# Kernel optimization log

Hardware: AMD Instinct MI355X
Metric: run time of the kernel (lower is better)

The kernel has to match this reference:

```python
import jax, jax.numpy as jnp
import numpy as np

SEQ, B, IN, H, L = 1024, 64, 256, 512, 2
EPS = 1e-5


def setup_inputs() -> dict:
    key = jax.random.key(0)
    ks = jax.random.split(key, 4)
    x = jax.random.normal(ks[0], (SEQ, B, IN), dtype=jnp.float32)
    h0 = jnp.zeros((L, B, H), dtype=jnp.float32)
    c0 = jnp.zeros((L, B, H), dtype=jnp.float32)
    # torch Linear weight layout: [4*H, in_features]
    W0 = jax.random.normal(ks[1], (4 * H, IN + H), dtype=jnp.float32) * 0.05
    b0 = jnp.zeros((4 * H,), dtype=jnp.float32)
    W1 = jax.random.normal(ks[2], (4 * H, H + H), dtype=jnp.float32) * 0.05
    b1 = jnp.zeros((4 * H,), dtype=jnp.float32)
    g0 = jnp.ones((H,), dtype=jnp.float32)
    beta0 = jnp.zeros((H,), dtype=jnp.float32)
    g1 = jnp.ones((H,), dtype=jnp.float32)
    beta1 = jnp.zeros((H,), dtype=jnp.float32)
    return {"x": x, "h0": h0, "c0": c0, "W0": W0, "b0": b0, "g0": g0,
            "beta0": beta0, "W1": W1, "b1": b1, "g1": g1, "beta1": beta1}


def _layer_norm(z, g, b):
    mu = jnp.mean(z, axis=-1, keepdims=True)
    var = jnp.mean(jnp.square(z - mu), axis=-1, keepdims=True)
    return (z - mu) * jax.lax.rsqrt(var + EPS) * g + b


def _cell(inp, h, c, W, b, g, beta):
    # gates: [B, 4H] via Linear on concat(x, h)
    gates = jnp.concatenate([inp, h], axis=-1) @ W.T + b
    i_t, f_t, o_t, cand = jnp.split(gates, 4, axis=-1)
    i_t = jax.nn.sigmoid(i_t)
    f_t = jax.nn.sigmoid(f_t)
    o_t = jax.nn.sigmoid(o_t)
    cand = jnp.tanh(cand)
    c_new = i_t * cand + f_t * c
    h_new = o_t * jnp.tanh(_layer_norm(c_new, g, beta))
    return h_new, c_new


def reference(x, h0, c0, W0, b0, g0, beta0, W1, b1, g1, beta1):
    def step(carry, xt):
        ha, ca, hb, cb = carry
        ha, ca = _cell(xt, ha, ca, W0, b0, g0, beta0)
        hb, cb = _cell(ha, hb, cb, W1, b1, g1, beta1)
        return (ha, ca, hb, cb), hb

    carry0 = (h0[0], c0[0], h0[1], c0[1])
    (ha, ca, hb, cb), outputs = jax.lax.scan(step, carry0, x)
    h_final = jnp.stack([ha, hb])  # [L, B, H]
    c_final = jnp.stack([ca, cb])
    return outputs, h_final, c_final
```

## Files before the change

kernel.cpp:

```cpp
#include <hip/hip_runtime.h>


typedef short  s16x8 __attribute__((ext_vector_type(8)));
typedef float  f32x4 __attribute__((ext_vector_type(4)));
typedef float  f32x2 __attribute__((ext_vector_type(2)));
typedef unsigned short u16;
typedef unsigned int   u32;

constexpr int kSeq = 1024;

constexpr size_t OF_FLAGS = 0;
constexpr size_t OF_PART0 = 1024;
constexpr size_t OF_PART1 = 33792;
constexpr size_t OF_HA    = 66560;
constexpr size_t OF_HB    = 197632;
constexpr size_t OF_W0S   = 328704;
constexpr size_t OF_W1S   = 3474432;
constexpr size_t OF_XBF   = 7668736;
constexpr size_t WS_NEED  = OF_XBF + 33554432;

constexpr size_t OUT_HFIN = (size_t)kSeq * 64 * 512;
constexpr size_t OUT_CFIN = OUT_HFIN + 2 * 64 * 512;

__device__ __forceinline__ u16 f2bf(float f) {
  u32 u = __float_as_uint(f);
  return (u16)((u + 0x7fffu + ((u >> 16) & 1u)) >> 16);
}

__device__ __forceinline__ void ldg16_coh(s16x8& d, const void* p) {
  asm volatile("global_load_dwordx4 %0, %1, off sc0 sc1" : "=v"(d) : "v"(p) : "memory");
}
__device__ __forceinline__ void ldg16f_coh(f32x4& d, const void* p) {
  asm volatile("global_load_dwordx4 %0, %1, off sc0 sc1" : "=v"(d) : "v"(p) : "memory");
}
__device__ __forceinline__ void stg8_coh(float* p, float a, float b) {
  f32x2 t; t[0] = a; t[1] = b;
  asm volatile("global_store_dwordx2 %0, %1, off sc0 sc1" :: "v"(p), "v"(t) : "memory");
}
__device__ __forceinline__ void stg2_coh(u16* p, u32 v) {
  asm volatile("global_store_short %0, %1, off sc0 sc1" :: "v"(p), "v"(v) : "memory");
}
__device__ __forceinline__ void vm_wait() {
  asm volatile("s_waitcnt vmcnt(0)" ::: "memory");
  __builtin_amdgcn_sched_barrier(0);
}
__device__ __forceinline__ void waitge(u32* f, u32 tgt) {
  const int l = threadIdx.x & 63;
  while (true) {
    u32 v = __hip_atomic_load(&f[l], __ATOMIC_RELAXED, __HIP_MEMORY_SCOPE_AGENT);
    if (__all((int)(v >= tgt))) break;
    __builtin_amdgcn_s_sleep(2);
  }
}

__global__ void conv_x_k(const float* __restrict__ x, u16* __restrict__ xd, size_t n) {
  size_t i = (size_t)blockIdx.x * blockDim.x + threadIdx.x;
  size_t st = (size_t)gridDim.x * blockDim.x;
  for (; i < n; i += st) xd[i] = f2bf(x[i]);
}

__global__ void conv_w_k(const float* __restrict__ W, u16* __restrict__ Wd,
                         int KST, int Kdim) {
  int i = blockIdx.x * blockDim.x + threadIdx.x;
  if (i >= 64 * KST * 1024) return;
  int e = i & 7, lane = (i >> 3) & 63, nt = (i >> 9) & 1;
  int r = i >> 10;
  int kst = r % KST, ns = r / KST;
  int lv = nt * 16 + (lane & 15);
  int n_orig = (lv >> 3) * 512 + ns * 8 + (lv & 7);
  int k = kst * 32 + ((lane >> 4) << 3) + e;
  Wd[i] = f2bf(W[(size_t)n_orig * Kdim + k]);
}

__global__ void init_k(char* ws, const float* __restrict__ h0) {
  int i = blockIdx.x * blockDim.x + threadIdx.x;
  u32* f = (u32*)ws;
  if (i < 256) f[i] = 0u;
  ((u16*)(ws + OF_HA))[32768 + i] = f2bf(h0[i]);
  ((u16*)(ws + OF_HB))[32768 + i] = f2bf(h0[32768 + i]);
}

template <int ROLE>
__device__ __forceinline__ void team_loop(
    int ns, char* smem,
    const u16* __restrict__ xbf, const u16* __restrict__ wsw,
    u16* hA, u16* hB, float* part, u32* flags,
    const float* __restrict__ bias, const float* __restrict__ gam_,
    const float* __restrict__ bet_, const float* __restrict__ c0in,
    float* __restrict__ out)
{
  constexpr int KST = ROLE ? 32 : 24;
  const int tid = threadIdx.x;
  const int lane = tid & 63, wid = tid >> 6;
  const int arow = wid * 16 + (lane & 15);
  const int acol = (lane >> 4) << 3;
  const int b1r = tid >> 3, jl = tid & 7, b2r = b1r + 32;
  const int jg = ns * 8 + jl;

  u32* HF0 = flags;
  u32* HF1 = flags + 64;
  u32* PF  = flags + 128 + ROLE * 64;
  u32* HF  = ROLE ? HF1 : HF0;

  s16x8* wl    = (s16x8*)smem;
  float* gates = (float*)(smem + 65536);
  float* mus   = (float*)(smem + 73728);

  const u16* wbase = wsw + (size_t)ns * KST * 1024;
  for (int i = tid; i < KST * 128; i += 256)
    wl[i] = *(const s16x8*)(wbase + (size_t)i * 8);

  const float bi = bias[jg], bf_ = bias[512 + jg], bo = bias[1024 + jg], bc = bias[1536 + jg];
  const float gm = gam_[jg], bt = bet_[jg];
  float cA = c0in[(size_t)(ROLE * 64 + b1r) * 512 + jg];
  float cB = c0in[(size_t)(ROLE * 64 + b2r) * 512 + jg];
  __syncthreads();

  for (int t = 0; t < kSeq; ++t) {
    f32x4 acc0 = {0.f, 0.f, 0.f, 0.f}, acc1 = {0.f, 0.f, 0.f, 0.f};

    auto mm = [&](s16x8 av, int kst) {
      acc0 = __builtin_amdgcn_mfma_f32_16x16x32_bf16(av, wl[(kst * 2) * 64 + lane], acc0, 0, 0, 0);
      acc1 = __builtin_amdgcn_mfma_f32_16x16x32_bf16(av, wl[(kst * 2 + 1) * 64 + lane], acc1, 0, 0, 0);
    };

    if (ROLE == 0) {
      s16x8 xp[8];
      const u16* xrow = xbf + ((size_t)t * 64 + arow) * 256 + acol;
      #pragma unroll
      for (int kk = 0; kk < 8; ++kk) xp[kk] = *(const s16x8*)(xrow + kk * 32);
      if (wid == 0)      { if (t > 0)  waitge(HF0, (u32)t); }
      else if (wid == 1) { if (t >= 2) waitge(HF1, (u32)(t - 1)); }
      __syncthreads();
      s16x8 a[16];
      const u16* hrow = hA + (size_t)((t + 1) & 1) * 32768 + (size_t)arow * 512 + acol;
      #pragma unroll
      for (int kk = 0; kk < 16; ++kk) ldg16_coh(a[kk], hrow + kk * 32);
      #pragma unroll
      for (int kk = 0; kk < 8; ++kk) mm(xp[kk], kk);
      vm_wait();
      #pragma unroll
      for (int kk = 0; kk < 16; ++kk) mm(a[kk], 8 + kk);
    } else {
      if (wid == 1) { if (t > 0) waitge(HF1, (u32)t); }
      __syncthreads();
      s16x8 a[16];
      const u16* hbrow = hB + (size_t)((t + 1) & 1) * 32768 + (size_t)arow * 512 + acol;
      #pragma unroll
      for (int kk = 0; kk < 16; ++kk) ldg16_coh(a[kk], hbrow + kk * 32);
      vm_wait();
      #pragma unroll
      for (int kk = 0; kk < 16; ++kk) mm(a[kk], 16 + kk);
      if (wid == 0) waitge(HF0, (u32)(t + 1));
      __syncthreads();
      const u16* harow = hA + (size_t)(t & 1) * 32768 + (size_t)arow * 512 + acol;
      #pragma unroll
      for (int kk = 0; kk < 16; ++kk) ldg16_coh(a[kk], harow + kk * 32);
      vm_wait();
      #pragma unroll
      for (int kk = 0; kk < 16; ++kk) mm(a[kk], kk);
    }

    #pragma unroll
    for (int r = 0; r < 4; ++r) {
      const int b = wid * 16 + ((lane >> 4) << 2) + r;
      gates[b * 32 + (lane & 15)]      = acc0[r];
      gates[b * 32 + 16 + (lane & 15)] = acc1[r];
    }
    __syncthreads();

    const float giA = gates[b1r * 32 + jl] + bi;
    const float gfA = gates[b1r * 32 + 8 + jl] + bf_;
    const float goA = gates[b1r * 32 + 16 + jl] + bo;
    const float gcA = gates[b1r * 32 + 24 + jl] + bc;
    const float giB = gates[b2r * 32 + jl] + bi;
    const float gfB = gates[b2r * 32 + 8 + jl] + bf_;
    const float goB = gates[b2r * 32 + 16 + jl] + bo;
    const float gcB = gates[b2r * 32 + 24 + jl] + bc;
    const float iA = 1.f / (1.f + __expf(-giA));
    const float fA = 1.f / (1.f + __expf(-gfA));
    const float oA = 1.f / (1.f + __expf(-goA));
    const float iB = 1.f / (1.f + __expf(-giB));
    const float fB = 1.f / (1.f + __expf(-gfB));
    const float oB = 1.f / (1.f + __expf(-goB));
    const float cnA = iA * tanhf(gcA) + fA * cA;
    const float cnB = iB * tanhf(gcB) + fB * cB;
    cA = cnA; cB = cnB;

    float s1 = cnA, q1 = cnA * cnA, s2 = cnB, q2 = cnB * cnB;
    #pragma unroll
    for (int m = 1; m <= 4; m <<= 1) {
      s1 += __shfl_xor(s1, m); q1 += __shfl_xor(q1, m);
      s2 += __shfl_xor(s2, m); q2 += __shfl_xor(q2, m);
    }
    if (jl == 0) {
      stg8_coh(part + ((size_t)b1r * 64 + ns) * 2, s1, q1);
      stg8_coh(part + ((size_t)b2r * 64 + ns) * 2, s2, q2);
    }
    vm_wait();
    __syncthreads();
    if (tid == 0)
      __hip_atomic_store(&PF[ns], (u32)(t + 1), __ATOMIC_RELAXED, __HIP_MEMORY_SCOPE_AGENT);
    if (wid == 0) waitge(PF, (u32)(t + 1));
    __syncthreads();
    if (tid < 64) {
      float ssum = 0.f, qsum = 0.f;
      const float* pr = part + (size_t)tid * 128;
      #pragma unroll
      for (int bch = 0; bch < 4; ++bch) {
        f32x4 gb[8];
        #pragma unroll
        for (int i2 = 0; i2 < 8; ++i2) ldg16f_coh(gb[i2], pr + (bch * 8 + i2) * 4);
        vm_wait();
        #pragma unroll
        for (int i2 = 0; i2 < 8; ++i2) { ssum += gb[i2][0] + gb[i2][2]; qsum += gb[i2][1] + gb[i2][3]; }
      }
      const float mu = ssum * (1.f / 512.f);
      const float ms = qsum * (1.f / 512.f);
      mus[tid * 2]     = mu;
      mus[tid * 2 + 1] = rsqrtf(ms - mu * mu + 1e-5f);
    }
    __syncthreads();
    const float muA = mus[b1r * 2], rsA = mus[b1r * 2 + 1];
    const float muB = mus[b2r * 2], rsB = mus[b2r * 2 + 1];
    const float hvA = oA * tanhf((cnA - muA) * rsA * gm + bt);
    const float hvB = oB * tanhf((cnB - muB) * rsB * gm + bt);
    const u32 ha16 = f2bf(hvA), hb16 = f2bf(hvB);

    u16* hd = (ROLE ? hB : hA) + (size_t)(t & 1) * 32768;
    stg2_coh(hd + (size_t)b1r * 512 + jg, ha16);
    stg2_coh(hd + (size_t)b2r * 512 + jg, hb16);
    if (ROLE == 1) {
      out[((size_t)t * 64 + b1r) * 512 + jg] = hvA;
      out[((size_t)t * 64 + b2r) * 512 + jg] = hvB;
    }
    if (t == kSeq - 1) {
      const size_t hb_ = OUT_HFIN + (size_t)ROLE * 32768;
      const size_t cb_ = OUT_CFIN + (size_t)ROLE * 32768;
      out[hb_ + (size_t)b1r * 512 + jg] = hvA;
      out[hb_ + (size_t)b2r * 512 + jg] = hvB;
      out[cb_ + (size_t)b1r * 512 + jg] = cnA;
      out[cb_ + (size_t)b2r * 512 + jg] = cnB;
    }
    vm_wait();
    __syncthreads();
    if (tid == 0)
      __hip_atomic_store(&HF[ns], (u32)(t + 1), __ATOMIC_RELAXED, __HIP_MEMORY_SCOPE_AGENT);
  }
}

__global__ __launch_bounds__(256, 1) void lstm_persist(
    const u16* __restrict__ xbf, const u16* __restrict__ w0s, const u16* __restrict__ w1s,
    char* ws,
    const float* __restrict__ b0, const float* __restrict__ lg0, const float* __restrict__ lb0,
    const float* __restrict__ b1, const float* __restrict__ lg1, const float* __restrict__ lb1,
    const float* __restrict__ c0in, float* __restrict__ out)
{
  extern __shared__ char smem[];
  const int bid = blockIdx.x;
  u32*   flags = (u32*)(ws + OF_FLAGS);
  u16*   hA    = (u16*)(ws + OF_HA);
  u16*   hB    = (u16*)(ws + OF_HB);
  float* p0    = (float*)(ws + OF_PART0);
  float* p1    = (float*)(ws + OF_PART1);

  if (bid < 64)
    team_loop<0>(bid, smem, xbf, w0s, hA, hB, p0, flags, b0, lg0, lb0, c0in, out);
  else
    team_loop<1>(bid - 64, smem, xbf, w1s, hA, hB, p1, flags, b1, lg1, lb1, c0in, out);
}

extern "C" void kernel_launch(void* const* d_in, const int* in_sizes, int n_in,
                              void* d_out, int out_size, void* d_ws, size_t ws_size,
                              hipStream_t stream) {
  (void)in_sizes; (void)n_in; (void)out_size;
  const float* x   = (const float*)d_in[0];
  const float* h0  = (const float*)d_in[1];
  const float* c0  = (const float*)d_in[2];
  const float* W0  = (const float*)d_in[3];
  const float* b0  = (const float*)d_in[4];
  const float* g0  = (const float*)d_in[5];
  const float* be0 = (const float*)d_in[6];
  const float* W1  = (const float*)d_in[7];
  const float* b1  = (const float*)d_in[8];
  const float* g1  = (const float*)d_in[9];
  const float* be1 = (const float*)d_in[10];
  float* out = (float*)d_out;

  if (ws_size < WS_NEED) return;

  char* ws = (char*)d_ws;
  u16* w0s = (u16*)(ws + OF_W0S);
  u16* w1s = (u16*)(ws + OF_W1S);
  u16* xbf = (u16*)(ws + OF_XBF);

  hipLaunchKernelGGL(conv_x_k, dim3(2048), dim3(256), 0, stream,
                     x, xbf, (size_t)kSeq * 64 * 256);
  hipLaunchKernelGGL(conv_w_k, dim3(6144), dim3(256), 0, stream, W0, w0s, 24, 768);
  hipLaunchKernelGGL(conv_w_k, dim3(8192), dim3(256), 0, stream, W1, w1s, 32, 1024);
  hipLaunchKernelGGL(init_k,   dim3(128),  dim3(256), 0, stream, ws, h0);
  hipLaunchKernelGGL(lstm_persist, dim3(128), dim3(256), 74240, stream,
                     xbf, w0s, w1s, ws,
                     b0, g0, be0, b1, g1, be1, c0, out);
}
```

Before: 15.41 ms.

## Halve persistent blocks and replace LayerNorm stats barrier with parity-tagged data

The persistent LSTM kernel now runs 64 blocks instead of 128, each owning 16 hidden units across four MFMA n-tiles, with the weight swizzle and LDS size doubled to match. The per-step LayerNorm partial-sum exchange drops its separate flag store and flag wait. The step parity is instead encoded in the sign bit of the sum-of-squares value, and readers poll the data directly until every entry carries the current parity. This is meant to cut one grid-wide synchronisation round per timestep and halve the number of blocks taking part in spin waits. The cost is twice the MFMA work and LDS footprint per block, and a correctness dependence on the sign-bit encoding.

```diff
diff --git a/kernel.cpp b/kernel.cpp
--- a/kernel.cpp
+++ b/kernel.cpp
@@ -6,17 +6,18 @@
 typedef float  f32x2 __attribute__((ext_vector_type(2)));
 typedef unsigned short u16;
 typedef unsigned int   u32;
+typedef unsigned long long u64;
 
 constexpr int kSeq = 1024;
 
 constexpr size_t OF_FLAGS = 0;
-constexpr size_t OF_PART0 = 1024;
-constexpr size_t OF_PART1 = 33792;
-constexpr size_t OF_HA    = 66560;
-constexpr size_t OF_HB    = 197632;
-constexpr size_t OF_W0S   = 328704;
-constexpr size_t OF_W1S   = 3474432;
-constexpr size_t OF_XBF   = 7668736;
+constexpr size_t OF_STAT0 = 1024;
+constexpr size_t OF_STAT1 = 17408;
+constexpr size_t OF_HA    = 33792;
+constexpr size_t OF_HB    = 164864;
+constexpr size_t OF_W0S   = 295936;
+constexpr size_t OF_W1S   = 3441664;
+constexpr size_t OF_XBF   = 7635968;
 constexpr size_t WS_NEED  = OF_XBF + 33554432;
 
 constexpr size_t OUT_HFIN = (size_t)kSeq * 64 * 512;
@@ -30,8 +31,8 @@
 __device__ __forceinline__ void ldg16_coh(s16x8& d, const void* p) {
   asm volatile("global_load_dwordx4 %0, %1, off sc0 sc1" : "=v"(d) : "v"(p) : "memory");
 }
-__device__ __forceinline__ void ldg16f_coh(f32x4& d, const void* p) {
-  asm volatile("global_load_dwordx4 %0, %1, off sc0 sc1" : "=v"(d) : "v"(p) : "memory");
+__device__ __forceinline__ void ldg8f_coh(f32x2& d, const void* p) {
+  asm volatile("global_load_dwordx2 %0, %1, off sc0 sc1" : "=v"(d) : "v"(p) : "memory");
 }
 __device__ __forceinline__ void stg8_coh(float* p, float a, float b) {
   f32x2 t; t[0] = a; t[1] = b;
@@ -45,7 +46,7 @@
   __builtin_amdgcn_sched_barrier(0);
 }
 __device__ __forceinline__ void waitge(u32* f, u32 tgt) {
-  const int l = threadIdx.x & 63;
+  const int l = threadIdx.x & 31;
   while (true) {
     u32 v = __hip_atomic_load(&f[l], __ATOMIC_RELAXED, __HIP_MEMORY_SCOPE_AGENT);
     if (__all((int)(v >= tgt))) break;
@@ -62,12 +63,11 @@
 __global__ void conv_w_k(const float* __restrict__ W, u16* __restrict__ Wd,
                          int KST, int Kdim) {
   int i = blockIdx.x * blockDim.x + threadIdx.x;
-  if (i >= 64 * KST * 1024) return;
-  int e = i & 7, lane = (i >> 3) & 63, nt = (i >> 9) & 1;
-  int r = i >> 10;
+  if (i >= 32 * KST * 2048) return;
+  int e = i & 7, lane = (i >> 3) & 63, nt = (i >> 9) & 3;
+  int r = i >> 11;
   int kst = r % KST, ns = r / KST;
-  int lv = nt * 16 + (lane & 15);
-  int n_orig = (lv >> 3) * 512 + ns * 8 + (lv & 7);
+  int n_orig = nt * 512 + ns * 16 + (lane & 15);
   int k = kst * 32 + ((lane >> 4) << 3) + e;
   Wd[i] = f2bf(W[(size_t)n_orig * Kdim + k]);
 }
@@ -75,7 +75,11 @@
 __global__ void init_k(char* ws, const float* __restrict__ h0) {
   int i = blockIdx.x * blockDim.x + threadIdx.x;
   u32* f = (u32*)ws;
-  if (i < 256) f[i] = 0u;
+  if (i < 64) f[i] = 0u;
+  if (i < 4096) {
+    ((u64*)(ws + OF_STAT0))[i] = 0x8000000000000000ull;
+    ((u64*)(ws + OF_STAT1))[i] = 0x8000000000000000ull;
+  }
   ((u16*)(ws + OF_HA))[32768 + i] = f2bf(h0[i]);
   ((u16*)(ws + OF_HB))[32768 + i] = f2bf(h0[32768 + i]);
 }
@@ -84,7 +88,7 @@
 __device__ __forceinline__ void team_loop(
     int ns, char* smem,
     const u16* __restrict__ xbf, const u16* __restrict__ wsw,
-    u16* hA, u16* hB, float* part, u32* flags,
+    u16* hA, u16* hB, float* statT, u32* flags,
     const float* __restrict__ bias, const float* __restrict__ gam_,
     const float* __restrict__ bet_, const float* __restrict__ c0in,
     float* __restrict__ out)
@@ -94,153 +98,163 @@
   const int lane = tid & 63, wid = tid >> 6;
   const int arow = wid * 16 + (lane & 15);
   const int acol = (lane >> 4) << 3;
-  const int b1r = tid >> 3, jl = tid & 7, b2r = b1r + 32;
-  const int jg = ns * 8 + jl;
-
-  u32* HF0 = flags;
-  u32* HF1 = flags + 64;
-  u32* PF  = flags + 128 + ROLE * 64;
-  u32* HF  = ROLE ? HF1 : HF0;
+  const int jl = tid & 15, rg = tid >> 4;
+  const int jg = ns * 16 + jl;
+
+  u32* HFA = flags;
+  u32* HF1 = flags + 32;
+  u32* HF  = ROLE ? HF1 : HFA;
 
   s16x8* wl    = (s16x8*)smem;
-  float* gates = (float*)(smem + 65536);
-  float* mus   = (float*)(smem + 73728);
-
-  const u16* wbase = wsw + (size_t)ns * KST * 1024;
-  for (int i = tid; i < KST * 128; i += 256)
-    wl[i] = *(const s16x8*)(wbase + (size_t)i * 8);
+  float* gates = (float*)(smem + (size_t)KST * 4096);
+  float* mus   = (float*)(smem + (size_t)KST * 4096 + 17408);
+
+  const s16x8* wsrc = (const s16x8*)wsw + (size_t)ns * KST * 256;
+  for (int i = tid; i < KST * 256; i += 256) wl[i] = wsrc[i];
 
   const float bi = bias[jg], bf_ = bias[512 + jg], bo = bias[1024 + jg], bc = bias[1536 + jg];
   const float gm = gam_[jg], bt = bet_[jg];
-  float cA = c0in[(size_t)(ROLE * 64 + b1r) * 512 + jg];
-  float cB = c0in[(size_t)(ROLE * 64 + b2r) * 512 + jg];
+  float cst[4];
+  #pragma unroll
+  for (int k = 0; k < 4; ++k)
+    cst[k] = c0in[(size_t)(ROLE * 64 + rg * 4 + k) * 512 + jg];
   __syncthreads();
 
   for (int t = 0; t < kSeq; ++t) {
-    f32x4 acc0 = {0.f, 0.f, 0.f, 0.f}, acc1 = {0.f, 0.f, 0.f, 0.f};
-
-    auto mm = [&](s16x8 av, int kst) {
-      acc0 = __builtin_amdgcn_mfma_f32_16x16x32_bf16(av, wl[(kst * 2) * 64 + lane], acc0, 0, 0, 0);
-      acc1 = __builtin_amdgcn_mfma_f32_16x16x32_bf16(av, wl[(kst * 2 + 1) * 64 + lane], acc1, 0, 0, 0);
-    };
+    f32x4 acc[4];
+    #pragma unroll
+    for (int nt = 0; nt < 4; ++nt) acc[nt] = (f32x4){0.f, 0.f, 0.f, 0.f};
 
     if (ROLE == 0) {
       s16x8 xp[8];
-      const u16* xrow = xbf + ((size_t)t * 64 + arow) * 256 + acol;
-      #pragma unroll
-      for (int kk = 0; kk < 8; ++kk) xp[kk] = *(const s16x8*)(xrow + kk * 32);
-      if (wid == 0)      { if (t > 0)  waitge(HF0, (u32)t); }
+      const u16* xr = xbf + ((size_t)t * 64 + arow) * 256 + acol;
+      #pragma unroll
+      for (int kk = 0; kk < 8; ++kk) xp[kk] = *(const s16x8*)(xr + kk * 32);
+      if (wid == 0)      { if (t > 0)  waitge(HFA, (u32)t); }
       else if (wid == 1) { if (t >= 2) waitge(HF1, (u32)(t - 1)); }
       __syncthreads();
       s16x8 a[16];
-      const u16* hrow = hA + (size_t)((t + 1) & 1) * 32768 + (size_t)arow * 512 + acol;
-      #pragma unroll
-      for (int kk = 0; kk < 16; ++kk) ldg16_coh(a[kk], hrow + kk * 32);
-      #pragma unroll
-      for (int kk = 0; kk < 8; ++kk) mm(xp[kk], kk);
+      const u16* hr = hA + (size_t)((t + 1) & 1) * 32768 + (size_t)arow * 512 + acol;
+      #pragma unroll
+      for (int kk = 0; kk < 16; ++kk) ldg16_coh(a[kk], hr + kk * 32);
+      #pragma unroll
+      for (int kk = 0; kk < 8; ++kk)
+        #pragma unroll
+        for (int nt = 0; nt < 4; ++nt)
+          acc[nt] = __builtin_amdgcn_mfma_f32_16x16x32_bf16(xp[kk], wl[(kk * 4 + nt) * 64 + lane], acc[nt], 0, 0, 0);
       vm_wait();
       #pragma unroll
-      for (int kk = 0; kk < 16; ++kk) mm(a[kk], 8 + kk);
+      for (int kk = 0; kk < 16; ++kk)
+        #pragma unroll
+        for (int nt = 0; nt < 4; ++nt)
+          acc[nt] = __builtin_amdgcn_mfma_f32_16x16x32_bf16(a[kk], wl[((8 + kk) * 4 + nt) * 64 + lane], acc[nt], 0, 0, 0);
     } else {
-      if (wid == 1) { if (t > 0) waitge(HF1, (u32)t); }
+      if (wid == 0) { if (t > 0) waitge(HF1, (u32)t); }
       __syncthreads();
       s16x8 a[16];
-      const u16* hbrow = hB + (size_t)((t + 1) & 1) * 32768 + (size_t)arow * 512 + acol;
-      #pragma unroll
-      for (int kk = 0; kk < 16; ++kk) ldg16_coh(a[kk], hbrow + kk * 32);
+      const u16* hbr = hB + (size_t)((t + 1) & 1) * 32768 + (size_t)arow * 512 + acol;
+      #pragma unroll
+      for (int kk = 0; kk < 16; ++kk) ldg16_coh(a[kk], hbr + kk * 32);
       vm_wait();
       #pragma unroll
-      for (int kk = 0; kk < 16; ++kk) mm(a[kk], 16 + kk);
-      if (wid == 0) waitge(HF0, (u32)(t + 1));
+      for (int kk = 0; kk < 16; ++kk)
+        #pragma unroll
+        for (int nt = 0; nt < 4; ++nt)
+          acc[nt] = __builtin_amdgcn_mfma_f32_16x16x32_bf16(a[kk], wl[((16 + kk) * 4 + nt) * 64 + lane], acc[nt], 0, 0, 0);
+      if (wid == 0) waitge(HFA, (u32)(t + 1));
       __syncthreads();
-      const u16* harow = hA + (size_t)(t & 1) * 32768 + (size_t)arow * 512 + acol;
-      #pragma unroll
-      for (int kk = 0; kk < 16; ++kk) ldg16_coh(a[kk], harow + kk * 32);
+      const u16* har = hA + (size_t)(t & 1) * 32768 + (size_t)arow * 512 + acol;
+      #pragma unroll
+      for (int kk = 0; kk < 16; ++kk) ldg16_coh(a[kk], har + kk * 32);
       vm_wait();
       #pragma unroll
-      for (int kk = 0; kk < 16; ++kk) mm(a[kk], kk);
-    }
-
-    #pragma unroll
-    for (int r = 0; r < 4; ++r) {
-      const int b = wid * 16 + ((lane >> 4) << 2) + r;
-      gates[b * 32 + (lane & 15)]      = acc0[r];
-      gates[b * 32 + 16 + (lane & 15)] = acc1[r];
+      for (int kk = 0; kk < 16; ++kk)
+        #pragma unroll
+        for (int nt = 0; nt < 4; ++nt)
+          acc[nt] = __builtin_amdgcn_mfma_f32_16x16x32_bf16(a[kk], wl[(kk * 4 + nt) * 64 + lane], acc[nt], 0, 0, 0);
+    }
+
+    #pragma unroll
+    for (int nt = 0; nt < 4; ++nt) {
+      const int brow = wid * 16 + ((lane >> 4) << 2);
+      #pragma unroll
+      for (int r = 0; r < 4; ++r)
+        gates[(nt * 64 + brow + r) * 17 + (lane & 15)] = acc[nt][r];
     }
     __syncthreads();
 
-    const float giA = gates[b1r * 32 + jl] + bi;
-    const float gfA = gates[b1r * 32 + 8 + jl] + bf_;
-    const float goA = gates[b1r * 32 + 16 + jl] + bo;
-    const float gcA = gates[b1r * 32 + 24 + jl] + bc;
-    const float giB = gates[b2r * 32 + jl] + bi;
-    const float gfB = gates[b2r * 32 + 8 + jl] + bf_;
-    const float goB = gates[b2r * 32 + 16 + jl] + bo;
-    const float gcB = gates[b2r * 32 + 24 + jl] + bc;
-    const float iA = 1.f / (1.f + __expf(-giA));
-    const float fA = 1.f / (1.f + __expf(-gfA));
-    const float oA = 1.f / (1.f + __expf(-goA));
-    const float iB = 1.f / (1.f + __expf(-giB));
-    const float fB = 1.f / (1.f + __expf(-gfB));
-    const float oB = 1.f / (1.f + __expf(-goB));
-    const float cnA = iA * tanhf(gcA) + fA * cA;
-    const float cnB = iB * tanhf(gcB) + fB * cB;
-    cA = cnA; cB = cnB;
-
-    float s1 = cnA, q1 = cnA * cnA, s2 = cnB, q2 = cnB * cnB;
-    #pragma unroll
-    for (int m = 1; m <= 4; m <<= 1) {
-      s1 += __shfl_xor(s1, m); q1 += __shfl_xor(q1, m);
-      s2 += __shfl_xor(s2, m); q2 += __shfl_xor(q2, m);
-    }
+    float cc[4], oo[4], sv[4], qv[4];
+    #pragma unroll
+    for (int k = 0; k < 4; ++k) {
+      const int row = rg * 4 + k;
+      const float gi = gates[(0 * 64 + row) * 17 + jl] + bi;
+      const float gf = gates[(1 * 64 + row) * 17 + jl] + bf_;
+      const float go = gates[(2 * 64 + row) * 17 + jl] + bo;
+      const float gc = gates[(3 * 64 + row) * 17 + jl] + bc;
+      const float iv = 1.f / (1.f + __expf(-gi));
+      const float fv = 1.f / (1.f + __expf(-gf));
+      oo[k] = 1.f / (1.f + __expf(-go));
+      const float cn = iv * tanhf(gc) + fv * cst[k];
+      cst[k] = cn; cc[k] = cn;
+      sv[k] = cn; qv[k] = cn * cn;
+    }
+    #pragma unroll
+    for (int m = 1; m <= 8; m <<= 1)
+      #pragma unroll
+      for (int k = 0; k < 4; ++k) { sv[k] += __shfl_xor(sv[k], m); qv[k] += __shfl_xor(qv[k], m); }
     if (jl == 0) {
-      stg8_coh(part + ((size_t)b1r * 64 + ns) * 2, s1, q1);
-      stg8_coh(part + ((size_t)b2r * 64 + ns) * 2, s2, q2);
-    }
-    vm_wait();
-    __syncthreads();
-    if (tid == 0)
-      __hip_atomic_store(&PF[ns], (u32)(t + 1), __ATOMIC_RELAXED, __HIP_MEMORY_SCOPE_AGENT);
-    if (wid == 0) waitge(PF, (u32)(t + 1));
-    __syncthreads();
-    if (tid < 64) {
-      float ssum = 0.f, qsum = 0.f;
-      const float* pr = part + (size_t)tid * 128;
-      #pragma unroll
-      for (int bch = 0; bch < 4; ++bch) {
-        f32x4 gb[8];
-        #pragma unroll
-        for (int i2 = 0; i2 < 8; ++i2) ldg16f_coh(gb[i2], pr + (bch * 8 + i2) * 4);
+      #pragma unroll
+      for (int k = 0; k < 4; ++k) {
+        const int row = rg * 4 + k;
+        const float qs = (t & 1) ? -qv[k] : qv[k];
+        stg8_coh(statT + ((size_t)row * 32 + ns) * 2, sv[k], qs);
+      }
+    }
+
+    {
+      const float* base = statT + (((size_t)(tid >> 2) * 32) + (size_t)(tid & 3) * 8) * 2;
+      const u32 want = (u32)(t & 1);
+      f32x2 e[8];
+      while (true) {
+        #pragma unroll
+        for (int j = 0; j < 8; ++j) ldg8f_coh(e[j], base + j * 2);
         vm_wait();
-        #pragma unroll
-        for (int i2 = 0; i2 < 8; ++i2) { ssum += gb[i2][0] + gb[i2][2]; qsum += gb[i2][1] + gb[i2][3]; }
-      }
-      const float mu = ssum * (1.f / 512.f);
-      const float ms = qsum * (1.f / 512.f);
-      mus[tid * 2]     = mu;
-      mus[tid * 2 + 1] = rsqrtf(ms - mu * mu + 1e-5f);
-    }
-    __syncthreads();
-    const float muA = mus[b1r * 2], rsA = mus[b1r * 2 + 1];
-    const float muB = mus[b2r * 2], rsB = mus[b2r * 2 + 1];
-    const float hvA = oA * tanhf((cnA - muA) * rsA * gm + bt);
-    const float hvB = oB * tanhf((cnB - muB) * rsB * gm + bt);
-    const u32 ha16 = f2bf(hvA), hb16 = f2bf(hvB);
-
-    u16* hd = (ROLE ? hB : hA) + (size_t)(t & 1) * 32768;
-    stg2_coh(hd + (size_t)b1r * 512 + jg, ha16);
-    stg2_coh(hd + (size_t)b2r * 512 + jg, hb16);
-    if (ROLE == 1) {
-      out[((size_t)t * 64 + b1r) * 512 + jg] = hvA;
-      out[((size_t)t * 64 + b2r) * 512 + jg] = hvB;
-    }
-    if (t == kSeq - 1) {
-      const size_t hb_ = OUT_HFIN + (size_t)ROLE * 32768;
-      const size_t cb_ = OUT_CFIN + (size_t)ROLE * 32768;
-      out[hb_ + (size_t)b1r * 512 + jg] = hvA;
-      out[hb_ + (size_t)b2r * 512 + jg] = hvB;
-      out[cb_ + (size_t)b1r * 512 + jg] = cnA;
-      out[cb_ + (size_t)b2r * 512 + jg] = cnB;
+        bool ok = true;
+        #pragma unroll
+        for (int j = 0; j < 8; ++j) ok &= ((__float_as_uint(e[j][1]) >> 31) == want);
+        if (__all((int)ok)) break;
+        __builtin_amdgcn_s_sleep(1);
+      }
+      float ss = 0.f, qq = 0.f;
+      #pragma unroll
+      for (int j = 0; j < 8; ++j) { ss += e[j][0]; qq += __builtin_fabsf(e[j][1]); }
+      ss += __shfl_xor(ss, 1); qq += __shfl_xor(qq, 1);
+      ss += __shfl_xor(ss, 2); qq += __shfl_xor(qq, 2);
+      if ((lane & 3) == 0) {
+        const int row = tid >> 2;
+        const float mu = ss * (1.f / 512.f);
+        const float ms = qq * (1.f / 512.f);
+        mus[row * 2] = mu;
+        mus[row * 2 + 1] = rsqrtf(ms - mu * mu + 1e-5f);
+      }
+    }
+
+    #pragma unroll
+    for (int k = 0; k < 4; ++k) {
+      const int row = rg * 4 + k;
+      const float mu = mus[row * 2], rs = mus[row * 2 + 1];
+      const float hv = oo[k] * tanhf((cc[k] - mu) * rs * gm + bt);
+      const u32 h16 = f2bf(hv);
+      if (ROLE == 0) {
+        stg2_coh(hA + (size_t)(t & 1) * 32768 + (size_t)row * 512 + jg, h16);
+      } else {
+        stg2_coh(hB + (size_t)(t & 1) * 32768 + (size_t)row * 512 + jg, h16);
+        out[((size_t)t * 64 + row) * 512 + jg] = hv;
+      }
+      if (t == kSeq - 1) {
+        out[OUT_HFIN + (size_t)ROLE * 32768 + (size_t)row * 512 + jg] = hv;
+        out[OUT_CFIN + (size_t)ROLE * 32768 + (size_t)row * 512 + jg] = cc[k];
+      }
     }
     vm_wait();
     __syncthreads();
@@ -261,13 +275,13 @@
   u32*   flags = (u32*)(ws + OF_FLAGS);
   u16*   hA    = (u16*)(ws + OF_HA);
   u16*   hB    = (u16*)(ws + OF_HB);
-  float* p0    = (float*)(ws + OF_PART0);
-  float* p1    = (float*)(ws + OF_PART1);
-
-  if (bid < 64)
-    team_loop<0>(bid, smem, xbf, w0s, hA, hB, p0, flags, b0, lg0, lb0, c0in, out);
+  float* st0   = (float*)(ws + OF_STAT0);
+  float* st1   = (float*)(ws + OF_STAT1);
+
+  if (bid < 32)
+    team_loop<0>(bid, smem, xbf, w0s, hA, hB, st0, flags, b0, lg0, lb0, c0in, out);
   else
-    team_loop<1>(bid - 64, smem, xbf, w1s, hA, hB, p1, flags, b1, lg1, lb1, c0in, out);
+    team_loop<1>(bid - 32, smem, xbf, w1s, hA, hB, st1, flags, b1, lg1, lb1, c0in, out);
 }
 
 extern "C" void kernel_launch(void* const* d_in, const int* in_sizes, int n_in,
@@ -299,7 +313,7 @@
   hipLaunchKernelGGL(conv_w_k, dim3(6144), dim3(256), 0, stream, W0, w0s, 24, 768);
   hipLaunchKernelGGL(conv_w_k, dim3(8192), dim3(256), 0, stream, W1, w1s, 32, 1024);
   hipLaunchKernelGGL(init_k,   dim3(128),  dim3(256), 0, stream, ws, h0);
-  hipLaunchKernelGGL(lstm_persist, dim3(128), dim3(256), 74240, stream,
+  hipLaunchKernelGGL(lstm_persist, dim3(64), dim3(256), 148992, stream,
                      xbf, w0s, w1s, ws,
                      b0, g0, be0, b1, g1, be1, c0, out);
 }
```

After: 15.83 ms. 1.03x slower.
